# Kernel tuning notes

Measured on AMD Instinct MI355X. Metric: run time of the kernel, lower is better.

## Reference

```python
import jax, jax.numpy as jnp
import numpy as np
import math

B, H, S, D = 2, 16, 2048, 64

def setup_inputs() -> dict:
    key = jax.random.key(0)
    kq, kk, kv = jax.random.split(key, 3)
    Q = jax.random.normal(kq, (B, H, S, D), dtype=jnp.float32)
    K = jax.random.normal(kk, (B, H, S, D), dtype=jnp.float32)
    V = jax.random.normal(kv, (B, H, S, D), dtype=jnp.float32)
    causal_mask = jnp.tril(jnp.ones((S, S), dtype=bool))
    return {"Q": Q, "K": K, "V": V, "causal_mask": causal_mask}

def reference(Q, K, V, causal_mask):
    d_k = K.shape[-1]
    scores = jnp.einsum('bhqd,bhkd->bhqk', Q, K) / math.sqrt(d_k)
    scores = jnp.where(causal_mask, scores, -jnp.inf)
    probs = jax.nn.softmax(scores, axis=-1)
    return jnp.einsum('bhqk,bhkd->bhqd', probs, V)
```

## Files before the change

kernel.cpp:

```cpp
#include <hip/hip_runtime.h>
#include <math.h>


constexpr int kS  = 2048;
constexpr int kD  = 64;
constexpr int kBH = 32;
constexpr int kPad = 72;
constexpr int kBQ  = 128;

typedef short short8 __attribute__((ext_vector_type(8)));
typedef float float4v __attribute__((ext_vector_type(4)));
typedef float float16v __attribute__((ext_vector_type(16)));
typedef unsigned short ushort4v __attribute__((ext_vector_type(4)));

static __device__ inline unsigned short f2bf(float f) {
  union { float f; unsigned u; } v; v.f = f;
  unsigned r = v.u + 0x7FFF + ((v.u >> 16) & 1);
  return (unsigned short)(r >> 16);
}

static __device__ inline short8 pack8(float4v a, float4v b) {
  short8 r;
  r[0] = (short)f2bf(a[0]); r[1] = (short)f2bf(a[1]);
  r[2] = (short)f2bf(a[2]); r[3] = (short)f2bf(a[3]);
  r[4] = (short)f2bf(b[0]); r[5] = (short)f2bf(b[1]);
  r[6] = (short)f2bf(b[2]); r[7] = (short)f2bf(b[3]);
  return r;
}

__global__ __launch_bounds__(256)
void prep_kernel(const float* __restrict__ K, const float* __restrict__ V,
                 unsigned short* __restrict__ Kb, unsigned short* __restrict__ VT) {
  __shared__ unsigned short tile[64 * kPad];
  const int tid = threadIdx.x;
  const int bh = blockIdx.y, st = blockIdx.x;
  const size_t ibase = (size_t)bh * kS * kD + (size_t)st * 64 * kD;
  const int r  = tid >> 2;
  const int c0 = (tid & 3) * 16;
  {
    const float* kp = K + ibase + (size_t)r * kD + c0;
    float4v a = *(const float4v*)(kp);
    float4v b = *(const float4v*)(kp + 4);
    float4v c = *(const float4v*)(kp + 8);
    float4v d = *(const float4v*)(kp + 12);
    unsigned short* dst = Kb + ibase + (size_t)r * kD + c0;
    *(short8*)dst       = pack8(a, b);
    *(short8*)(dst + 8) = pack8(c, d);
  }
  {
    const float* vp = V + ibase + (size_t)r * kD + c0;
    float4v a = *(const float4v*)(vp);
    float4v b = *(const float4v*)(vp + 4);
    float4v c = *(const float4v*)(vp + 8);
    float4v d = *(const float4v*)(vp + 12);
    unsigned short* t = &tile[r * kPad + c0];
    *(short8*)t       = pack8(a, b);
    *(short8*)(t + 8) = pack8(c, d);
  }
  __syncthreads();
  {
    const int dd = tid >> 2;
    const int s0 = (tid & 3) * 16;
    short8 w0, w1;
    #pragma unroll
    for (int i = 0; i < 8; ++i) {
      w0[i] = (short)tile[(s0 + i) * kPad + dd];
      w1[i] = (short)tile[(s0 + 8 + i) * kPad + dd];
    }
    unsigned short* vdst = VT + (size_t)bh * kD * kS + (size_t)dd * kS + st * 64 + s0;
    *(short8*)vdst       = w0;
    *(short8*)(vdst + 8) = w1;
  }
}

__global__ __launch_bounds__(256)
void fattn_kernel(const float* __restrict__ Q, const unsigned short* __restrict__ Kb,
                  const unsigned short* __restrict__ VT, float* __restrict__ O) {
  __shared__ __align__(16) unsigned short ldsK[64 * kPad];
  __shared__ __align__(16) unsigned short ldsVT[64 * kPad];
  __shared__ __align__(16) unsigned short ldsP[4 * 32 * kPad];
  __shared__ float ldsL[4 * 32];

  const int tid  = threadIdx.x;
  const int wave = tid >> 6;
  const int lane = tid & 63;
  const int l31  = lane & 31;
  const int h    = lane >> 5;

  const int bh = blockIdx.y;
  const int qi = gridDim.x - 1 - blockIdx.x;
  const int q0 = qi * kBQ;
  const int wq0 = q0 + wave * 32;

  const size_t base = (size_t)bh * kS * kD;

  short8 qf[4];
  {
    const float scl = 0.125f * 1.44269504089f;
    const float* qp = Q + base + (size_t)(wq0 + l31) * kD + h * 8;
    #pragma unroll
    for (int dk = 0; dk < 4; ++dk) {
      float4v a = *(const float4v*)(qp + dk * 16);
      float4v b = *(const float4v*)(qp + dk * 16 + 4);
      #pragma unroll
      for (int i = 0; i < 4; ++i) { a[i] *= scl; b[i] *= scl; }
      qf[dk] = pack8(a, b);
    }
  }

  float16v acc0, acc1;
  #pragma unroll
  for (int i = 0; i < 16; ++i) { acc0[i] = 0.f; acc1[i] = 0.f; }
  float lacc = 0.f;

  const int srow = tid >> 2;
  const int sc0  = (tid & 3) * 16;
  const unsigned short* Kg = Kb + base + (size_t)srow * kD + sc0;
  const unsigned short* Vg = VT + (size_t)bh * kD * kS + (size_t)srow * kS + sc0;

  const int nkt = 2 * qi + 2;

  short8 pk0 = *(const short8*)(Kg);
  short8 pk1 = *(const short8*)(Kg + 8);
  short8 pv0 = *(const short8*)(Vg);
  short8 pv1 = *(const short8*)(Vg + 8);

  unsigned short* pw = &ldsP[wave * 32 * kPad + l31 * kPad];

  for (int kt = 0; kt < nkt; ++kt) {
    const int kb = kt * 64;
    __syncthreads();
    {
      unsigned short* kd = &ldsK[srow * kPad + sc0];
      *(short8*)kd       = pk0;
      *(short8*)(kd + 8) = pk1;
      unsigned short* vd = &ldsVT[srow * kPad + sc0];
      *(short8*)vd       = pv0;
      *(short8*)(vd + 8) = pv1;
    }
    __syncthreads();
    if (kt + 1 < nkt) {
      Kg += 64 * kD;
      Vg += 64;
      pk0 = *(const short8*)(Kg);
      pk1 = *(const short8*)(Kg + 8);
      pv0 = *(const short8*)(Vg);
      pv1 = *(const short8*)(Vg + 8);
    }

    #pragma unroll
    for (int kt32 = 0; kt32 < 2; ++kt32) {
      const int ktb = kb + kt32 * 32;
      if (ktb > wq0 + 31) break;

      float16v s;
      #pragma unroll
      for (int i = 0; i < 16; ++i) s[i] = 0.f;
      const unsigned short* kro = &ldsK[(kt32 * 32 + l31) * kPad + h * 8];
      #pragma unroll
      for (int dk = 0; dk < 4; ++dk) {
        short8 kf = *(const short8*)(kro + dk * 16);
        s = __builtin_amdgcn_mfma_f32_32x32x16_bf16(kf, qf[dk], s, 0, 0, 0);
      }

      if (ktb + 31 > wq0) {
        const int qg = wq0 + l31;
        #pragma unroll
        for (int r = 0; r < 16; ++r) {
          const int kg = ktb + (r & 3) + 8 * (r >> 2) + 4 * h;
          if (kg > qg) s[r] = -1e30f;
        }
      }

      #pragma unroll
      for (int rb = 0; rb < 4; ++rb) {
        ushort4v w;
        #pragma unroll
        for (int i = 0; i < 4; ++i) {
          float p = __builtin_amdgcn_exp2f(s[rb * 4 + i]);
          lacc += p;
          w[i] = (unsigned short)(__float_as_uint(p) >> 16);
        }
        *(ushort4v*)(pw + kt32 * 32 + rb * 8 + 4 * h) = w;
      }

      #pragma unroll
      for (int kc2 = 0; kc2 < 2; ++kc2) {
        const int ko = kt32 * 32 + kc2 * 16;
        short8 pf  = *(const short8*)(pw + ko + h * 8);
        short8 vf0 = *(const short8*)(&ldsVT[l31 * kPad + ko + h * 8]);
        short8 vf1 = *(const short8*)(&ldsVT[(32 + l31) * kPad + ko + h * 8]);
        acc0 = __builtin_amdgcn_mfma_f32_32x32x16_bf16(pf, vf0, acc0, 0, 0, 0);
        acc1 = __builtin_amdgcn_mfma_f32_32x32x16_bf16(pf, vf1, acc1, 0, 0, 0);
      }
    }
  }

  lacc += __shfl_xor(lacc, 32);
  if (h == 0) ldsL[wave * 32 + l31] = lacc;
  __syncthreads();
  #pragma unroll
  for (int r = 0; r < 16; ++r) {
    const int row = (r & 3) + 8 * (r >> 2) + 4 * h;
    const float inv = 1.f / ldsL[wave * 32 + row];
    const int qg = wq0 + row;
    float* op = O + base + (size_t)qg * kD + l31;
    op[0]  = acc0[r] * inv;
    op[32] = acc1[r] * inv;
  }
}

extern "C" void kernel_launch(void* const* d_in, const int* in_sizes, int n_in,
                              void* d_out, int out_size, void* d_ws, size_t ws_size,
                              hipStream_t stream) {
  const float* Q = (const float*)d_in[0];
  const float* K = (const float*)d_in[1];
  const float* V = (const float*)d_in[2];
  float* O = (float*)d_out;

  unsigned short* Kb = (unsigned short*)d_ws;
  unsigned short* VT = Kb + (size_t)kBH * kS * kD;

  dim3 gprep(kS / 64, kBH);
  prep_kernel<<<gprep, 256, 0, stream>>>(K, V, Kb, VT);
  dim3 grid(kS / kBQ, kBH);
  fattn_kernel<<<grid, 256, 0, stream>>>(Q, Kb, VT, O);
}
```

Measured before the change: 150.1 us.

## Split each query tile's KV range across two blocks and combine partials

Each query tile's causal key range is split into two halves, and each half is processed by its own block, doubling the grid from 512 to 1024 blocks to improve occupancy and load balance on the many CUs. Unnormalized partial outputs and row sums go to the output and a workspace buffer. A new combine kernel adds the partials and normalizes them. This works without a running max because the scores are never max-subtracted. The cost is an extra launch plus extra global traffic for the partial O, the row sums and the combine pass.

```diff
diff --git a/kernel.cpp b/kernel.cpp
--- a/kernel.cpp
+++ b/kernel.cpp
@@ -2,11 +2,12 @@
 #include <math.h>
 
 
-constexpr int kS  = 2048;
-constexpr int kD  = 64;
-constexpr int kBH = 32;
+constexpr int kS   = 2048;
+constexpr int kD   = 64;
+constexpr int kBH  = 32;
 constexpr int kPad = 72;
 constexpr int kBQ  = 128;
+constexpr int kNQI = kS / kBQ;
 
 typedef short short8 __attribute__((ext_vector_type(8)));
 typedef float float4v __attribute__((ext_vector_type(4)));
@@ -75,11 +76,12 @@
 
 __global__ __launch_bounds__(256)
 void fattn_kernel(const float* __restrict__ Q, const unsigned short* __restrict__ Kb,
-                  const unsigned short* __restrict__ VT, float* __restrict__ O) {
+                  const unsigned short* __restrict__ VT,
+                  float* __restrict__ O0, float* __restrict__ O1,
+                  float* __restrict__ Lp) {
   __shared__ __align__(16) unsigned short ldsK[64 * kPad];
   __shared__ __align__(16) unsigned short ldsVT[64 * kPad];
   __shared__ __align__(16) unsigned short ldsP[4 * 32 * kPad];
-  __shared__ float ldsL[4 * 32];
 
   const int tid  = threadIdx.x;
   const int wave = tid >> 6;
@@ -88,7 +90,9 @@
   const int h    = lane >> 5;
 
   const int bh = blockIdx.y;
-  const int qi = gridDim.x - 1 - blockIdx.x;
+  const int bx = blockIdx.x;
+  const int qi = (kNQI - 1) - (bx >> 1);
+  const int z  = bx & 1;
   const int q0 = qi * kBQ;
   const int wq0 = q0 + wave * 32;
 
@@ -113,12 +117,14 @@
   for (int i = 0; i < 16; ++i) { acc0[i] = 0.f; acc1[i] = 0.f; }
   float lacc = 0.f;
 
+  const int tBeg = z * (qi + 1);
+  const int tEnd = tBeg + (qi + 1);
+
   const int srow = tid >> 2;
   const int sc0  = (tid & 3) * 16;
-  const unsigned short* Kg = Kb + base + (size_t)srow * kD + sc0;
-  const unsigned short* Vg = VT + (size_t)bh * kD * kS + (size_t)srow * kS + sc0;
-
-  const int nkt = 2 * qi + 2;
+  const unsigned short* Kg = Kb + base + (size_t)(tBeg * 64 + srow) * kD + sc0;
+  const unsigned short* Vg = VT + (size_t)bh * kD * kS + (size_t)srow * kS
+                                + tBeg * 64 + sc0;
 
   short8 pk0 = *(const short8*)(Kg);
   short8 pk1 = *(const short8*)(Kg + 8);
@@ -127,7 +133,7 @@
 
   unsigned short* pw = &ldsP[wave * 32 * kPad + l31 * kPad];
 
-  for (int kt = 0; kt < nkt; ++kt) {
+  for (int kt = tBeg; kt < tEnd; ++kt) {
     const int kb = kt * 64;
     __syncthreads();
     {
@@ -139,7 +145,7 @@
       *(short8*)(vd + 8) = pv1;
     }
     __syncthreads();
-    if (kt + 1 < nkt) {
+    if (kt + 1 < tEnd) {
       Kg += 64 * kD;
       Vg += 64;
       pk0 = *(const short8*)(Kg);
@@ -197,17 +203,30 @@
   }
 
   lacc += __shfl_xor(lacc, 32);
-  if (h == 0) ldsL[wave * 32 + l31] = lacc;
-  __syncthreads();
+  if (h == 0) Lp[(size_t)z * kBH * kS + (size_t)bh * kS + wq0 + l31] = lacc;
+
+  float* Od = z ? O1 : O0;
   #pragma unroll
   for (int r = 0; r < 16; ++r) {
     const int row = (r & 3) + 8 * (r >> 2) + 4 * h;
-    const float inv = 1.f / ldsL[wave * 32 + row];
-    const int qg = wq0 + row;
-    float* op = O + base + (size_t)qg * kD + l31;
-    op[0]  = acc0[r] * inv;
-    op[32] = acc1[r] * inv;
-  }
+    float* op = Od + base + (size_t)(wq0 + row) * kD + l31;
+    op[0]  = acc0[r];
+    op[32] = acc1[r];
+  }
+}
+
+__global__ __launch_bounds__(256)
+void combine_kernel(const float* __restrict__ O1, const float* __restrict__ Lp,
+                    float* __restrict__ O) {
+  const int idx4 = blockIdx.x * 256 + threadIdx.x;
+  const int row  = idx4 >> 4;
+  const float l  = Lp[row] + Lp[kBH * kS + row];
+  const float inv = 1.f / l;
+  float4v a = ((const float4v*)O)[idx4];
+  float4v b = ((const float4v*)O1)[idx4];
+  #pragma unroll
+  for (int i = 0; i < 4; ++i) a[i] = (a[i] + b[i]) * inv;
+  ((float4v*)O)[idx4] = a;
 }
 
 extern "C" void kernel_launch(void* const* d_in, const int* in_sizes, int n_in,
@@ -218,11 +237,16 @@
   const float* V = (const float*)d_in[2];
   float* O = (float*)d_out;
 
+  const size_t nKV = (size_t)kBH * kS * kD;
   unsigned short* Kb = (unsigned short*)d_ws;
-  unsigned short* VT = Kb + (size_t)kBH * kS * kD;
+  unsigned short* VT = Kb + nKV;
+  float* O1 = (float*)(VT + nKV);
+  float* Lp = O1 + nKV;
 
   dim3 gprep(kS / 64, kBH);
   prep_kernel<<<gprep, 256, 0, stream>>>(K, V, Kb, VT);
-  dim3 grid(kS / kBQ, kBH);
-  fattn_kernel<<<grid, 256, 0, stream>>>(Q, Kb, VT, O);
-}
+  dim3 grid(kNQI * 2, kBH);
+  fattn_kernel<<<grid, 256, 0, stream>>>(Q, Kb, VT, O, O1, Lp);
+  const int n4 = (int)(nKV / 4);
+  combine_kernel<<<n4 / 256, 256, 0, stream>>>(O1, Lp, O);
+}
```

Measured after the change: 149.8 us. Within noise of the previous version (-0.2%).
